# Performance work log

Hardware: AMD Instinct MI355X
Metric: run time of the kernel (lower is better)

Reference implementation:

```python
import jax, jax.numpy as jnp
import numpy as np

EPS = 1e-8  # torch F.cosine_similarity eps


def setup_inputs() -> dict:
    key = jax.random.key(0)
    k1, k2, k3 = jax.random.split(key, 3)
    bn, cn, dim = 4096, 8192, 1024
    x = jax.random.normal(k1, (bn, dim), dtype=jnp.float32)
    positive = jax.random.normal(k2, (bn, dim), dtype=jnp.float32)
    negative = jax.random.normal(k3, (cn, dim), dtype=jnp.float32)
    return {"x": x, "positive": positive, "negative": negative}


def reference(x, positive, negative):
    bn = x.shape[0]
    nx = jnp.linalg.norm(x, axis=1)          # (bn,)
    npos = jnp.linalg.norm(positive, axis=1)  # (bn,)
    nneg = jnp.linalg.norm(negative, axis=1)  # (cn,)
    # positive cosine similarity, torch-style eps clamp on norm product
    sim = jnp.sum(x * positive, axis=1) / jnp.maximum(nx * npos, EPS)  # (bn,)
    # negative cosine similarities via one matmul instead of (bn,cn,dim) repeats
    neg_sim = (x @ negative.T) / jnp.maximum(nx[:, None] * nneg[None, :], EPS)  # (bn,cn)
    p = jnp.exp(sim) / jnp.sum(jnp.exp(neg_sim), axis=1)  # (bn,)
    loss = -jnp.sum(jnp.log(p)) / bn
    return loss
```

## Files before the change

kernel.cpp:

```cpp
#include <hip/hip_runtime.h>
#include <stdint.h>
#include <stddef.h>

#define DIM 1024
#define EPS 1e-8f

typedef __attribute__((ext_vector_type(4)))  int   i32x4;
typedef __attribute__((ext_vector_type(8)))  int   i32x8;
typedef __attribute__((ext_vector_type(4)))  float f32x4;

#define SCALE8 0x7B7B7B7B

__device__ __forceinline__ void async_copy16(const void* g, void* l) {
    __builtin_amdgcn_global_load_lds(
        (__attribute__((address_space(1))) void*)const_cast<void*>(g),
        (__attribute__((address_space(3))) void*)(l), 16, 0, 0);
}

__global__ __launch_bounds__(256)
void prep_all(const float* __restrict__ x, const float* __restrict__ pos,
              const float* __restrict__ neg,
              unsigned char* __restrict__ Xn, unsigned char* __restrict__ Nn,
              float* __restrict__ simOut, float* __restrict__ rowsum, int bn) {
    const int lane = threadIdx.x & 63;
    const int wave = threadIdx.x >> 6;
    const int grow = blockIdx.x * 4 + wave;
    const bool isX = grow < bn;
    const int row  = isX ? grow : grow - bn;
    const float* src = isX ? x : neg;
    unsigned char* dst = isX ? Xn : Nn;

    const float4* s = (const float4*)(src + (size_t)row * DIM);
    float4 xv[4], pv[4];
    float sxx = 0.f, spp = 0.f, sxp = 0.f;
#pragma unroll
    for (int i = 0; i < 4; i++) {
        xv[i] = s[lane + 64 * i];
        sxx += xv[i].x * xv[i].x + xv[i].y * xv[i].y + xv[i].z * xv[i].z + xv[i].w * xv[i].w;
    }
    if (isX) {
        const float4* p = (const float4*)(pos + (size_t)row * DIM);
#pragma unroll
        for (int i = 0; i < 4; i++) {
            pv[i] = p[lane + 64 * i];
            spp += pv[i].x * pv[i].x + pv[i].y * pv[i].y + pv[i].z * pv[i].z + pv[i].w * pv[i].w;
            sxp += xv[i].x * pv[i].x + xv[i].y * pv[i].y + xv[i].z * pv[i].z + xv[i].w * pv[i].w;
        }
#pragma unroll
        for (int off = 1; off < 64; off <<= 1) {
            sxx += __shfl_xor(sxx, off);
            spp += __shfl_xor(spp, off);
            sxp += __shfl_xor(sxp, off);
        }
    } else {
#pragma unroll
        for (int off = 1; off < 64; off <<= 1) sxx += __shfl_xor(sxx, off);
    }
    const float nx  = sqrtf(sxx);
    const float inv = (nx > 0.f) ? (16.f / nx) : 0.f;
    if (isX && lane == 0) {
        const float np = sqrtf(spp);
        simOut[row] = sxp / fmaxf(nx * np, EPS);
        rowsum[row] = 0.f;
    }
    unsigned int t;
    t = __builtin_amdgcn_cvt_pk_fp8_f32(xv[0].x * inv, xv[0].y * inv, 0, false);
    unsigned int q0 = __builtin_amdgcn_cvt_pk_fp8_f32(xv[0].z * inv, xv[0].w * inv, t, true);
    t = __builtin_amdgcn_cvt_pk_fp8_f32(xv[1].x * inv, xv[1].y * inv, 0, false);
    unsigned int q1 = __builtin_amdgcn_cvt_pk_fp8_f32(xv[1].z * inv, xv[1].w * inv, t, true);
    t = __builtin_amdgcn_cvt_pk_fp8_f32(xv[2].x * inv, xv[2].y * inv, 0, false);
    unsigned int q2 = __builtin_amdgcn_cvt_pk_fp8_f32(xv[2].z * inv, xv[2].w * inv, t, true);
    t = __builtin_amdgcn_cvt_pk_fp8_f32(xv[3].x * inv, xv[3].y * inv, 0, false);
    unsigned int q3 = __builtin_amdgcn_cvt_pk_fp8_f32(xv[3].z * inv, xv[3].w * inv, t, true);

    unsigned int* wr = (unsigned int*)(dst + (size_t)row * DIM);
    wr[lane]       = q0;
    wr[lane + 64]  = q1;
    wr[lane + 128] = q2;
    wr[lane + 192] = q3;
}

__global__ __launch_bounds__(512, 2)
void gemm_exp_rowsum(const unsigned char* __restrict__ Xn,
                     const unsigned char* __restrict__ Nn,
                     float* __restrict__ rowsum) {
    constexpr int KB   = DIM;
    constexpr int BK   = 128;
    constexpr int BUFB = 256 * BK + 128 * BK;
    constexpr int BOFF = 256 * BK;
    extern __shared__ unsigned char smem[];

    const int tid  = threadIdx.x;
    const int lane = tid & 63;
    const int wave = tid >> 6;

    const int nwg  = gridDim.x * gridDim.y;
    const int bid  = blockIdx.y * gridDim.x + blockIdx.x;
    const int swz  = (bid & 7) * (nwg >> 3) + (bid >> 3);
    const int rowBase = (swz / gridDim.x) * 256;
    const int colBase = (swz % gridDim.x) * 128;

    const int srow = lane >> 3;
    const int sch  = (lane & 7) ^ srow;
    const unsigned char* gA = Xn + (size_t)(rowBase + wave * 32 + srow) * KB + sch * 16;
    const unsigned char* gB = Nn + (size_t)(colBase + wave * 16 + srow) * KB + sch * 16;

    const f32x4 fz = {0.f, 0.f, 0.f, 0.f};
    f32x4 acc[4][4];
#pragma unroll
    for (int mi = 0; mi < 4; mi++)
#pragma unroll
        for (int ni = 0; ni < 4; ni++) acc[mi][ni] = fz;

    const int m0   = (wave >> 1) * 64;
    const int n0   = (wave & 1) * 64;
    const int mrow = lane & 15;
    const int q    = lane >> 4;
    const int c0   = ((2 * q) ^ (mrow & 7)) << 4;

    int aoff[4], boff[4];
#pragma unroll
    for (int i = 0; i < 4; i++) {
        aoff[i] = (m0 + 16 * i + mrow) * BK + c0;
        boff[i] = BOFF + (n0 + 16 * i + mrow) * BK + c0;
    }

#define STAGE_HALF(buf, stg, h)                                                \
    do {                                                                       \
        const int kq = (stg) * BK;                                             \
        unsigned char* Lb = smem + (buf) * BUFB;                               \
        async_copy16(gA + (size_t)(16 * (h)) * KB + kq,                        \
                     Lb + (wave * 32 + 16 * (h)) * BK);                        \
        async_copy16(gA + (size_t)(16 * (h) + 8) * KB + kq,                    \
                     Lb + (wave * 32 + 16 * (h) + 8) * BK);                    \
        async_copy16(gB + (size_t)(8 * (h)) * KB + kq,                         \
                     Lb + BOFF + (wave * 16 + 8 * (h)) * BK);                  \
    } while (0)

#define RD(base, off, dst)                                                     \
    do {                                                                       \
        i32x4 lo_ = *(const i32x4*)((base) + (off));                           \
        i32x4 hi_ = *(const i32x4*)((base) + ((off) ^ 16));                    \
        dst = __builtin_shufflevector(lo_, hi_, 0, 1, 2, 3, 4, 5, 6, 7);       \
    } while (0)

    STAGE_HALF(0, 0, 0);
    STAGE_HALF(0, 0, 1);
    STAGE_HALF(1, 1, 0);
    STAGE_HALF(1, 1, 1);
    asm volatile("s_waitcnt vmcnt(6)\n\ts_barrier" ::: "memory");

#pragma unroll
    for (int w = 0; w < 8; w++) {
        const int b  = w % 3;
        const int nb = (w + 2) % 3;
        const unsigned char* Ab = smem + b * BUFB;
        i32x8 Af[4], Bf[2];
        if (w < 6) STAGE_HALF(nb, w + 2, 0);
#pragma unroll
        for (int i = 0; i < 4; i++) RD(Ab, aoff[i], Af[i]);
#pragma unroll
        for (int i = 0; i < 2; i++) RD(Ab, boff[i], Bf[i]);
        __builtin_amdgcn_s_setprio(1);
#pragma unroll
        for (int mi = 0; mi < 4; mi++)
#pragma unroll
            for (int ni = 0; ni < 2; ni++)
                acc[mi][ni] = __builtin_amdgcn_mfma_scale_f32_16x16x128_f8f6f4(
                    Af[mi], Bf[ni], acc[mi][ni], 0, 0, 0, SCALE8, 0, SCALE8);
        __builtin_amdgcn_s_setprio(0);
        asm volatile("s_barrier" ::: "memory");
        if (w < 6) STAGE_HALF(nb, w + 2, 1);
#pragma unroll
        for (int i = 0; i < 2; i++) RD(Ab, boff[2 + i], Bf[i]);
        __builtin_amdgcn_s_setprio(1);
#pragma unroll
        for (int mi = 0; mi < 4; mi++)
#pragma unroll
            for (int ni = 0; ni < 2; ni++)
                acc[mi][2 + ni] = __builtin_amdgcn_mfma_scale_f32_16x16x128_f8f6f4(
                    Af[mi], Bf[ni], acc[mi][2 + ni], 0, 0, 0, SCALE8, 0, SCALE8);
        __builtin_amdgcn_s_setprio(0);
        if (w < 6) {
            asm volatile("s_waitcnt vmcnt(6)\n\ts_barrier" ::: "memory");
        } else if (w == 6) {
            asm volatile("s_waitcnt vmcnt(0)\n\ts_barrier" ::: "memory");
        }
    }
#undef STAGE_HALF
#undef RD

#pragma unroll
    for (int mi = 0; mi < 4; mi++) {
        float rs0 = 0.f, rs1 = 0.f, rs2 = 0.f, rs3 = 0.f;
#pragma unroll
        for (int ni = 0; ni < 4; ni++) {
            rs0 += __expf(acc[mi][ni].x);
            rs1 += __expf(acc[mi][ni].y);
            rs2 += __expf(acc[mi][ni].z);
            rs3 += __expf(acc[mi][ni].w);
        }
#pragma unroll
        for (int off = 1; off < 16; off <<= 1) {
            rs0 += __shfl_xor(rs0, off);
            rs1 += __shfl_xor(rs1, off);
            rs2 += __shfl_xor(rs2, off);
            rs3 += __shfl_xor(rs3, off);
        }
        if ((lane & 15) == 0) {
            const int r = rowBase + m0 + mi * 16 + q * 4;
            atomicAdd(&rowsum[r + 0], rs0);
            atomicAdd(&rowsum[r + 1], rs1);
            atomicAdd(&rowsum[r + 2], rs2);
            atomicAdd(&rowsum[r + 3], rs3);
        }
    }
}

__global__ __launch_bounds__(1024)
void loss_kernel(const float* __restrict__ rowsum, const float* __restrict__ sim,
                 float* __restrict__ out, int bn) {
    const int tid  = threadIdx.x;
    const int lane = tid & 63;
    const int wave = tid >> 6;
    float acc = 0.f;
    for (int i = tid; i < bn; i += 1024) acc += logf(rowsum[i]) - sim[i];
#pragma unroll
    for (int off = 1; off < 64; off <<= 1) acc += __shfl_xor(acc, off);
    __shared__ float red[16];
    if (lane == 0) red[wave] = acc;
    __syncthreads();
    if (tid == 0) {
        float t = 0.f;
#pragma unroll
        for (int i = 0; i < 16; i++) t += red[i];
        out[0] = t / (float)bn;
    }
}

extern "C" void kernel_launch(void* const* d_in, const int* in_sizes, int n_in,
                              void* d_out, int out_size, void* d_ws, size_t ws_size,
                              hipStream_t stream) {
    const float* x   = (const float*)d_in[0];
    const float* pos = (const float*)d_in[1];
    const float* neg = (const float*)d_in[2];
    const int bn = in_sizes[0] / DIM;
    const int cn = in_sizes[2] / DIM;

    unsigned char* Xn = (unsigned char*)d_ws;
    unsigned char* Nn = Xn + (size_t)bn * DIM;
    float* sim    = (float*)(Nn + (size_t)cn * DIM);
    float* rowsum = sim + bn;

    static bool attr_done = false;
    if (!attr_done) {
        (void)hipFuncSetAttribute((const void*)gemm_exp_rowsum,
                                  hipFuncAttributeMaxDynamicSharedMemorySize,
                                  147456);
        attr_done = true;
    }

    prep_all<<<dim3((bn + cn) / 4), dim3(256), 0, stream>>>(x, pos, neg, Xn, Nn, sim, rowsum, bn);
    gemm_exp_rowsum<<<dim3(cn / 128, bn / 256), dim3(512), 147456, stream>>>(Xn, Nn, rowsum);
    loss_kernel<<<dim3(1), dim3(1024), 0, stream>>>(rowsum, sim, (float*)d_out, bn);
}
```

Measured before the change: 157.0 us.

## Enlarge GEMM tile to 256x256 with double-buffered full-stage loads

Changes the FP8 GEMM workgroup tile from 256x128 to 256x256. Each wave now computes a 128x64 sub-tile with 32 accumulators, which raises arithmetic intensity and halves how often A tiles are refetched. The triple-buffered half-stage pipeline is replaced by a simpler double buffer that loads a full K stage at a time and waits on vmcnt(0) before every barrier. This shortens the prefetch distance and may expose load latency. The doubled accumulator count also raises register pressure under launch_bounds(512,2), and 131072 bytes of LDS per block likely allows only one block per CU.

```diff
diff --git a/kernel.cpp b/kernel.cpp
--- a/kernel.cpp
+++ b/kernel.cpp
@@ -86,8 +86,8 @@
                      float* __restrict__ rowsum) {
     constexpr int KB   = DIM;
     constexpr int BK   = 128;
-    constexpr int BUFB = 256 * BK + 128 * BK;
     constexpr int BOFF = 256 * BK;
+    constexpr int BUFB = 2 * BOFF;
     extern __shared__ unsigned char smem[];
 
     const int tid  = threadIdx.x;
@@ -98,43 +98,43 @@
     const int bid  = blockIdx.y * gridDim.x + blockIdx.x;
     const int swz  = (bid & 7) * (nwg >> 3) + (bid >> 3);
     const int rowBase = (swz / gridDim.x) * 256;
-    const int colBase = (swz % gridDim.x) * 128;
+    const int colBase = (swz % gridDim.x) * 256;
 
     const int srow = lane >> 3;
     const int sch  = (lane & 7) ^ srow;
     const unsigned char* gA = Xn + (size_t)(rowBase + wave * 32 + srow) * KB + sch * 16;
-    const unsigned char* gB = Nn + (size_t)(colBase + wave * 16 + srow) * KB + sch * 16;
+    const unsigned char* gB = Nn + (size_t)(colBase + wave * 32 + srow) * KB + sch * 16;
 
     const f32x4 fz = {0.f, 0.f, 0.f, 0.f};
-    f32x4 acc[4][4];
-#pragma unroll
-    for (int mi = 0; mi < 4; mi++)
+    f32x4 acc[8][4];
+#pragma unroll
+    for (int mi = 0; mi < 8; mi++)
 #pragma unroll
         for (int ni = 0; ni < 4; ni++) acc[mi][ni] = fz;
 
-    const int m0   = (wave >> 1) * 64;
-    const int n0   = (wave & 1) * 64;
+    const int m0   = (wave >> 2) * 128;
+    const int n0   = (wave & 3) * 64;
     const int mrow = lane & 15;
     const int q    = lane >> 4;
     const int c0   = ((2 * q) ^ (mrow & 7)) << 4;
 
-    int aoff[4], boff[4];
-#pragma unroll
-    for (int i = 0; i < 4; i++) {
-        aoff[i] = (m0 + 16 * i + mrow) * BK + c0;
-        boff[i] = BOFF + (n0 + 16 * i + mrow) * BK + c0;
-    }
-
-#define STAGE_HALF(buf, stg, h)                                                \
+    int aoff[8], boff[4];
+#pragma unroll
+    for (int i = 0; i < 8; i++) aoff[i] = (m0 + 16 * i + mrow) * BK + c0;
+#pragma unroll
+    for (int i = 0; i < 4; i++) boff[i] = BOFF + (n0 + 16 * i + mrow) * BK + c0;
+
+#define STAGE(buf, stg)                                                        \
     do {                                                                       \
         const int kq = (stg) * BK;                                             \
         unsigned char* Lb = smem + (buf) * BUFB;                               \
-        async_copy16(gA + (size_t)(16 * (h)) * KB + kq,                        \
-                     Lb + (wave * 32 + 16 * (h)) * BK);                        \
-        async_copy16(gA + (size_t)(16 * (h) + 8) * KB + kq,                    \
-                     Lb + (wave * 32 + 16 * (h) + 8) * BK);                    \
-        async_copy16(gB + (size_t)(8 * (h)) * KB + kq,                         \
-                     Lb + BOFF + (wave * 16 + 8 * (h)) * BK);                  \
+        _Pragma("unroll")                                                      \
+        for (int i = 0; i < 4; i++) {                                          \
+            async_copy16(gA + (size_t)(8 * i) * KB + kq,                       \
+                         Lb + (wave * 32 + 8 * i) * BK);                       \
+            async_copy16(gB + (size_t)(8 * i) * KB + kq,                       \
+                         Lb + BOFF + (wave * 32 + 8 * i) * BK);                \
+        }                                                                      \
     } while (0)
 
 #define RD(base, off, dst)                                                     \
@@ -144,54 +144,35 @@
         dst = __builtin_shufflevector(lo_, hi_, 0, 1, 2, 3, 4, 5, 6, 7);       \
     } while (0)
 
-    STAGE_HALF(0, 0, 0);
-    STAGE_HALF(0, 0, 1);
-    STAGE_HALF(1, 1, 0);
-    STAGE_HALF(1, 1, 1);
-    asm volatile("s_waitcnt vmcnt(6)\n\ts_barrier" ::: "memory");
+    STAGE(0, 0);
+    asm volatile("s_waitcnt vmcnt(0)\n\ts_barrier" ::: "memory");
 
 #pragma unroll
     for (int w = 0; w < 8; w++) {
-        const int b  = w % 3;
-        const int nb = (w + 2) % 3;
-        const unsigned char* Ab = smem + b * BUFB;
-        i32x8 Af[4], Bf[2];
-        if (w < 6) STAGE_HALF(nb, w + 2, 0);
-#pragma unroll
-        for (int i = 0; i < 4; i++) RD(Ab, aoff[i], Af[i]);
-#pragma unroll
-        for (int i = 0; i < 2; i++) RD(Ab, boff[i], Bf[i]);
-        __builtin_amdgcn_s_setprio(1);
-#pragma unroll
-        for (int mi = 0; mi < 4; mi++)
-#pragma unroll
-            for (int ni = 0; ni < 2; ni++)
+        const unsigned char* Ab = smem + (w & 1) * BUFB;
+        if (w < 7) STAGE((w + 1) & 1, w + 1);
+        i32x8 Bf[4];
+#pragma unroll
+        for (int i = 0; i < 4; i++) RD(Ab, boff[i], Bf[i]);
+#pragma unroll
+        for (int mi = 0; mi < 8; mi++) {
+            i32x8 Af;
+            RD(Ab, aoff[mi], Af);
+            __builtin_amdgcn_s_setprio(1);
+#pragma unroll
+            for (int ni = 0; ni < 4; ni++)
                 acc[mi][ni] = __builtin_amdgcn_mfma_scale_f32_16x16x128_f8f6f4(
-                    Af[mi], Bf[ni], acc[mi][ni], 0, 0, 0, SCALE8, 0, SCALE8);
-        __builtin_amdgcn_s_setprio(0);
-        asm volatile("s_barrier" ::: "memory");
-        if (w < 6) STAGE_HALF(nb, w + 2, 1);
-#pragma unroll
-        for (int i = 0; i < 2; i++) RD(Ab, boff[2 + i], Bf[i]);
-        __builtin_amdgcn_s_setprio(1);
-#pragma unroll
-        for (int mi = 0; mi < 4; mi++)
-#pragma unroll
-            for (int ni = 0; ni < 2; ni++)
-                acc[mi][2 + ni] = __builtin_amdgcn_mfma_scale_f32_16x16x128_f8f6f4(
-                    Af[mi], Bf[ni], acc[mi][2 + ni], 0, 0, 0, SCALE8, 0, SCALE8);
-        __builtin_amdgcn_s_setprio(0);
-        if (w < 6) {
-            asm volatile("s_waitcnt vmcnt(6)\n\ts_barrier" ::: "memory");
-        } else if (w == 6) {
+                    Af, Bf[ni], acc[mi][ni], 0, 0, 0, SCALE8, 0, SCALE8);
+            __builtin_amdgcn_s_setprio(0);
+        }
+        if (w < 7)
             asm volatile("s_waitcnt vmcnt(0)\n\ts_barrier" ::: "memory");
-        }
-    }
-#undef STAGE_HALF
+    }
+#undef STAGE
 #undef RD
 
 #pragma unroll
-    for (int mi = 0; mi < 4; mi++) {
+    for (int mi = 0; mi < 8; mi++) {
         float rs0 = 0.f, rs1 = 0.f, rs2 = 0.f, rs3 = 0.f;
 #pragma unroll
         for (int ni = 0; ni < 4; ni++) {
@@ -256,11 +237,11 @@
     if (!attr_done) {
         (void)hipFuncSetAttribute((const void*)gemm_exp_rowsum,
                                   hipFuncAttributeMaxDynamicSharedMemorySize,
-                                  147456);
+                                  131072);
         attr_done = true;
     }
 
     prep_all<<<dim3((bn + cn) / 4), dim3(256), 0, stream>>>(x, pos, neg, Xn, Nn, sim, rowsum, bn);
-    gemm_exp_rowsum<<<dim3(cn / 128, bn / 256), dim3(512), 147456, stream>>>(Xn, Nn, rowsum);
+    gemm_exp_rowsum<<<dim3(cn / 256, bn / 256), dim3(512), 131072, stream>>>(Xn, Nn, rowsum);
     loss_kernel<<<dim3(1), dim3(1024), 0, stream>>>(rowsum, sim, (float*)d_out, bn);
 }
```

Result: slower. 252.5 us (+60.8%).

## Split GEMM k-step into four MFMA phases and remap blocks per XCD

Applied to the files above, without the earlier changes.

The main loop is restructured from two phases of 8 MFMAs into four phases of 4 MFMAs. Each phase issues a smaller batch of async global-to-LDS loads and only the LDS fragment reads it needs, with a barrier between phases. This spreads memory traffic more evenly across the MFMA stream. The block swizzle is also changed so that each XCD owns a compact 8x16 tile region of the output, which should improve L2 reuse of the A and B panels. In exchange the kernel takes more barriers per k-step and holds all four B fragments at once, which raises register pressure.

```diff
diff --git a/kernel.cpp b/kernel.cpp
--- a/kernel.cpp
+++ b/kernel.cpp
@@ -86,19 +86,21 @@
                      float* __restrict__ rowsum) {
     constexpr int KB   = DIM;
     constexpr int BK   = 128;
-    constexpr int BUFB = 256 * BK + 128 * BK;
     constexpr int BOFF = 256 * BK;
+    constexpr int BUFB = BOFF + 128 * BK;
     extern __shared__ unsigned char smem[];
 
     const int tid  = threadIdx.x;
     const int lane = tid & 63;
     const int wave = tid >> 6;
 
-    const int nwg  = gridDim.x * gridDim.y;
     const int bid  = blockIdx.y * gridDim.x + blockIdx.x;
-    const int swz  = (bid & 7) * (nwg >> 3) + (bid >> 3);
-    const int rowBase = (swz / gridDim.x) * 256;
-    const int colBase = (swz % gridDim.x) * 128;
+    const int xcd  = bid & 7;
+    const int idx  = bid >> 3;
+    const int brow = (xcd >> 2) * 8  + (idx >> 4);
+    const int bcol = (xcd &  3) * 16 + (idx & 15);
+    const int rowBase = brow * 256;
+    const int colBase = bcol * 128;
 
     const int srow = lane >> 3;
     const int sch  = (lane & 7) ^ srow;
@@ -125,17 +127,12 @@
         boff[i] = BOFF + (n0 + 16 * i + mrow) * BK + c0;
     }
 
-#define STAGE_HALF(buf, stg, h)                                                \
-    do {                                                                       \
-        const int kq = (stg) * BK;                                             \
-        unsigned char* Lb = smem + (buf) * BUFB;                               \
-        async_copy16(gA + (size_t)(16 * (h)) * KB + kq,                        \
-                     Lb + (wave * 32 + 16 * (h)) * BK);                        \
-        async_copy16(gA + (size_t)(16 * (h) + 8) * KB + kq,                    \
-                     Lb + (wave * 32 + 16 * (h) + 8) * BK);                    \
-        async_copy16(gB + (size_t)(8 * (h)) * KB + kq,                         \
-                     Lb + BOFF + (wave * 16 + 8 * (h)) * BK);                  \
-    } while (0)
+#define STAGE_A(buf, stg, h)                                                   \
+    async_copy16(gA + (size_t)(8 * (h)) * KB + (stg) * BK,                     \
+                 smem + (buf) * BUFB + (wave * 32 + 8 * (h)) * BK)
+#define STAGE_B(buf, stg, h)                                                   \
+    async_copy16(gB + (size_t)(8 * (h)) * KB + (stg) * BK,                     \
+                 smem + (buf) * BUFB + BOFF + (wave * 16 + 8 * (h)) * BK)
 
 #define RD(base, off, dst)                                                     \
     do {                                                                       \
@@ -144,51 +141,63 @@
         dst = __builtin_shufflevector(lo_, hi_, 0, 1, 2, 3, 4, 5, 6, 7);       \
     } while (0)
 
-    STAGE_HALF(0, 0, 0);
-    STAGE_HALF(0, 0, 1);
-    STAGE_HALF(1, 1, 0);
-    STAGE_HALF(1, 1, 1);
+#define MFMA4(MI0, NI0)                                                        \
+    do {                                                                       \
+        __builtin_amdgcn_s_setprio(1);                                         \
+        _Pragma("unroll")                                                      \
+        for (int mi_ = 0; mi_ < 2; mi_++)                                      \
+            _Pragma("unroll")                                                  \
+            for (int ni_ = 0; ni_ < 2; ni_++)                                  \
+                acc[(MI0) + mi_][(NI0) + ni_] =                                \
+                    __builtin_amdgcn_mfma_scale_f32_16x16x128_f8f6f4(          \
+                        Af[(MI0) + mi_], Bf[(NI0) + ni_],                      \
+                        acc[(MI0) + mi_][(NI0) + ni_], 0, 0, 0,                \
+                        SCALE8, 0, SCALE8);                                    \
+        __builtin_amdgcn_s_setprio(0);                                         \
+    } while (0)
+
+#define PH_BAR() asm volatile("s_barrier" ::: "memory")
+
+#pragma unroll
+    for (int h = 0; h < 4; h++) { STAGE_A(0, 0, h); }
+    STAGE_B(0, 0, 0); STAGE_B(0, 0, 1);
+#pragma unroll
+    for (int h = 0; h < 4; h++) { STAGE_A(1, 1, h); }
+    STAGE_B(1, 1, 0); STAGE_B(1, 1, 1);
     asm volatile("s_waitcnt vmcnt(6)\n\ts_barrier" ::: "memory");
 
 #pragma unroll
     for (int w = 0; w < 8; w++) {
         const int b  = w % 3;
         const int nb = (w + 2) % 3;
-        const unsigned char* Ab = smem + b * BUFB;
-        i32x8 Af[4], Bf[2];
-        if (w < 6) STAGE_HALF(nb, w + 2, 0);
-#pragma unroll
-        for (int i = 0; i < 4; i++) RD(Ab, aoff[i], Af[i]);
-#pragma unroll
-        for (int i = 0; i < 2; i++) RD(Ab, boff[i], Bf[i]);
-        __builtin_amdgcn_s_setprio(1);
-#pragma unroll
-        for (int mi = 0; mi < 4; mi++)
-#pragma unroll
-            for (int ni = 0; ni < 2; ni++)
-                acc[mi][ni] = __builtin_amdgcn_mfma_scale_f32_16x16x128_f8f6f4(
-                    Af[mi], Bf[ni], acc[mi][ni], 0, 0, 0, SCALE8, 0, SCALE8);
-        __builtin_amdgcn_s_setprio(0);
-        asm volatile("s_barrier" ::: "memory");
-        if (w < 6) STAGE_HALF(nb, w + 2, 1);
-#pragma unroll
-        for (int i = 0; i < 2; i++) RD(Ab, boff[2 + i], Bf[i]);
-        __builtin_amdgcn_s_setprio(1);
-#pragma unroll
-        for (int mi = 0; mi < 4; mi++)
-#pragma unroll
-            for (int ni = 0; ni < 2; ni++)
-                acc[mi][2 + ni] = __builtin_amdgcn_mfma_scale_f32_16x16x128_f8f6f4(
-                    Af[mi], Bf[ni], acc[mi][2 + ni], 0, 0, 0, SCALE8, 0, SCALE8);
-        __builtin_amdgcn_s_setprio(0);
+        const unsigned char* Lb = smem + b * BUFB;
+        i32x8 Af[4], Bf[4];
+        if (w < 6) { STAGE_A(nb, w + 2, 0); STAGE_A(nb, w + 2, 1); }
+        RD(Lb, aoff[0], Af[0]); RD(Lb, aoff[1], Af[1]);
+        RD(Lb, boff[0], Bf[0]); RD(Lb, boff[1], Bf[1]);
+        MFMA4(0, 0);
+        PH_BAR();
+        if (w < 6) { STAGE_A(nb, w + 2, 2); STAGE_A(nb, w + 2, 3); }
+        RD(Lb, boff[2], Bf[2]); RD(Lb, boff[3], Bf[3]);
+        MFMA4(0, 2);
+        PH_BAR();
+        if (w < 6) STAGE_B(nb, w + 2, 0);
+        RD(Lb, aoff[2], Af[2]); RD(Lb, aoff[3], Af[3]);
+        MFMA4(2, 0);
+        PH_BAR();
+        if (w < 6) STAGE_B(nb, w + 2, 1);
+        MFMA4(2, 2);
         if (w < 6) {
             asm volatile("s_waitcnt vmcnt(6)\n\ts_barrier" ::: "memory");
         } else if (w == 6) {
             asm volatile("s_waitcnt vmcnt(0)\n\ts_barrier" ::: "memory");
         }
     }
-#undef STAGE_HALF
+#undef STAGE_A
+#undef STAGE_B
 #undef RD
+#undef MFMA4
+#undef PH_BAR
 
 #pragma unroll
     for (int mi = 0; mi < 4; mi++) {
```

Result: slower. 171.8 us (+9.4%).
